# Performance work log

Hardware: AMD Instinct MI355X
Metric: run time of the kernel (lower is better)

The kernel has to match this reference:

```python
import jax, jax.numpy as jnp
import numpy as np

IMPOSSIBLE = -10000.0
TAGSET_SIZE = 64
NUM_TAGS = TAGSET_SIZE + 2  # C = 66
START_IDX = NUM_TAGS - 2
STOP_IDX = NUM_TAGS - 1
B, L, D = 32, 1024, 1024


def setup_inputs() -> dict:
    key = jax.random.key(0)
    k1, k2, k3, k4, k5 = jax.random.split(key, 5)
    features = jax.random.normal(k1, (B, L, D), dtype=jnp.float32)
    ys = jax.random.randint(k2, (B, L), 0, TAGSET_SIZE).astype(jnp.int64)
    masks = jnp.ones((B, L), dtype=jnp.float32)
    fc_w = jax.random.normal(k3, (D, NUM_TAGS), dtype=jnp.float32) / np.sqrt(D)
    fc_b = jax.random.normal(k4, (NUM_TAGS,), dtype=jnp.float32) * 0.01
    transitions = jax.random.normal(k5, (NUM_TAGS, NUM_TAGS), dtype=jnp.float32)
    # transitions TO start and FROM stop are impossible (torch indexing [to, from])
    transitions = transitions.at[START_IDX, :].set(IMPOSSIBLE)
    transitions = transitions.at[:, STOP_IDX].set(IMPOSSIBLE)
    return {"features": features, "ys": ys, "masks": masks,
            "fc_w": fc_w, "fc_b": fc_b, "transitions": transitions}


def _forward_algorithm(feats, masks, transitions):
    """CRF partition function. feats: [B,L,C], masks: [B,L] -> [B]."""
    Bb, Ll, C = feats.shape
    scores0 = jnp.full((Bb, C), IMPOSSIBLE, dtype=feats.dtype).at[:, START_IDX].set(0.0)

    def step(scores, xs):
        emit_t, m_t = xs  # emit_t: [B,C], m_t: [B]
        # score_t[b, j] = logsumexp_i( scores[b,i] + trans[j,i] + emit[b,j] )
        score_t = jax.nn.logsumexp(
            scores[:, None, :] + transitions[None, :, :] + emit_t[:, :, None], axis=-1)
        scores = score_t * m_t[:, None] + scores * (1.0 - m_t[:, None])
        return scores, None

    xs = (jnp.swapaxes(feats, 0, 1), jnp.swapaxes(masks, 0, 1))  # [L,B,C], [L,B]
    scores, _ = jax.lax.scan(step, scores0, xs)
    return jax.nn.logsumexp(scores + transitions[STOP_IDX][None, :], axis=-1)


def _score_sentence(feats, tags, masks, transitions):
    """Score of the gold tag path. feats: [B,L,C], tags: [B,L] -> [B]."""
    Bb, Ll, C = feats.shape
    emit = jnp.take_along_axis(feats, tags[:, :, None], axis=2)[:, :, 0]  # [B,L]
    start = jnp.full((Bb, 1), START_IDX, dtype=tags.dtype)
    tags_ext = jnp.concatenate([start, tags], axis=1)  # [B,L+1]
    trans_sc = transitions[tags_ext[:, 1:], tags_ext[:, :-1]]  # [B,L]
    lengths = masks.sum(1).astype(jnp.int32)  # [B]
    last_tag = tags_ext[jnp.arange(Bb), lengths]  # [B]
    last_score = transitions[STOP_IDX, last_tag]
    return ((trans_sc + emit) * masks).sum(1) + last_score


def reference(features, ys, masks, fc_w, fc_b, transitions):
    feats = jnp.einsum('bld,dc->blc', features, fc_w) + fc_b  # [B,L,C]
    masks_ = masks.astype(feats.dtype)
    forward_score = _forward_algorithm(feats, masks_, transitions)  # [B]
    gold_score = _score_sentence(feats, ys.astype(jnp.int32), masks_, transitions)  # [B]
    return (forward_score, gold_score)
```

## Files before the change

kernel.cpp:

```cpp
#include <hip/hip_runtime.h>
#include <hip/hip_bf16.h>
#include <stdint.h>


#define START_IDX 64
#define STOP_IDX 65
#define LN2F 0.6931471805599453f

typedef __attribute__((ext_vector_type(4))) float f32x4;
typedef __attribute__((ext_vector_type(8))) __bf16 bf16x8;
typedef __attribute__((ext_vector_type(4))) __bf16 bf16x4;

template <int CTRL>
__device__ __forceinline__ float dpp_mov(float v) {
  return __int_as_float(
      __builtin_amdgcn_update_dpp(0, __float_as_int(v), CTRL, 0xF, 0xF, true));
}
__device__ __forceinline__ float wave_max64(float v) {
  v = fmaxf(v, dpp_mov<0xB1>(v));
  v = fmaxf(v, dpp_mov<0x4E>(v));
  v = fmaxf(v, dpp_mov<0x141>(v));
  v = fmaxf(v, dpp_mov<0x140>(v));
  v = fmaxf(v, dpp_mov<0x142>(v));
  v = fmaxf(v, dpp_mov<0x143>(v));
  return v;
}
__device__ __forceinline__ float wave_sum64(float v) {
  v += dpp_mov<0xB1>(v);
  v += dpp_mov<0x4E>(v);
  v += dpp_mov<0x141>(v);
  v += dpp_mov<0x140>(v);
  v += dpp_mov<0x142>(v);
  v += dpp_mov<0x143>(v);
  return v;
}

__global__ void crf_wcvt(const float* __restrict__ W,
                         unsigned short* __restrict__ Wbt) {
  const int idx = blockIdx.x * 256 + threadIdx.x;
  const int n = idx >> 10, k = idx & 1023;
  union { __bf16 h; unsigned short u; } cv;
  cv.h = (__bf16)W[k * 66 + n];
  Wbt[idx] = cv.u;
}

__global__ __launch_bounds__(256) void crf_mm(const float* __restrict__ A,
                                              const unsigned short* __restrict__ Wbt,
                                              const float* __restrict__ bias,
                                              float* __restrict__ out) {
  const int tid = threadIdx.x;
  const int w = tid >> 6, lane = tid & 63, g = lane >> 4, q = lane & 15;
  const int m0 = blockIdx.x * 64 + 16 * w;

  const float* Arow = A + (size_t)(m0 + q) * 1024 + 8 * g;
  const unsigned short* Bp0 = Wbt + (q + 0) * 1024 + 8 * g;
  const unsigned short* Bp1 = Wbt + (q + 16) * 1024 + 8 * g;
  const unsigned short* Bp2 = Wbt + (q + 32) * 1024 + 8 * g;
  const unsigned short* Bp3 = Wbt + (q + 48) * 1024 + 8 * g;

  f32x4 acc0 = {0.f, 0.f, 0.f, 0.f}, acc1 = acc0, acc2 = acc0, acc3 = acc0;

#pragma unroll
  for (int k0 = 0; k0 < 1024; k0 += 32) {
    float4 a0 = *(const float4*)(Arow + k0);
    float4 a1 = *(const float4*)(Arow + k0 + 4);
    bf16x8 af;
    af[0] = (__bf16)a0.x; af[1] = (__bf16)a0.y; af[2] = (__bf16)a0.z; af[3] = (__bf16)a0.w;
    af[4] = (__bf16)a1.x; af[5] = (__bf16)a1.y; af[6] = (__bf16)a1.z; af[7] = (__bf16)a1.w;
    bf16x8 b0 = *(const bf16x8*)(Bp0 + k0);
    bf16x8 b1 = *(const bf16x8*)(Bp1 + k0);
    bf16x8 b2 = *(const bf16x8*)(Bp2 + k0);
    bf16x8 b3 = *(const bf16x8*)(Bp3 + k0);
    acc0 = __builtin_amdgcn_mfma_f32_16x16x32_bf16(af, b0, acc0, 0, 0, 0);
    acc1 = __builtin_amdgcn_mfma_f32_16x16x32_bf16(af, b1, acc1, 0, 0, 0);
    acc2 = __builtin_amdgcn_mfma_f32_16x16x32_bf16(af, b2, acc2, 0, 0, 0);
    acc3 = __builtin_amdgcn_mfma_f32_16x16x32_bf16(af, b3, acc3, 0, 0, 0);
  }

  const float bb0 = bias[q + 0], bb1 = bias[q + 16];
  const float bb2 = bias[q + 32], bb3 = bias[q + 48];
#pragma unroll
  for (int r = 0; r < 4; ++r) {
    float* orow = out + (size_t)(m0 + 4 * g + r) * 64 + q;
    orow[0]  = acc0[r] + bb0;
    orow[16] = acc1[r] + bb1;
    orow[32] = acc2[r] + bb2;
    orow[48] = acc3[r] + bb3;
  }
}

__global__ __launch_bounds__(256) void crf_chunks(const float* __restrict__ feats,
                                                  const float* __restrict__ masks,
                                                  const float* __restrict__ trans,
                                                  float* __restrict__ chunkP,
                                                  int* __restrict__ chunkExp) {
  __shared__ __align__(16) unsigned short T[2][4096];
  __shared__ float wmax[2][4];
  const int tid = threadIdx.x;
  const int w = tid >> 6, lane = tid & 63, g = lane >> 4, q = lane & 15;
  const int c = blockIdx.x, b = blockIdx.y;
  const int t0 = (c == 0) ? 1 : (c << 6);
  const int t1 = (c << 6) + 64;

  bf16x8 Ea0, Ea1;
  {
    const int i = 16 * w + q;
    const float* tp0 = trans + i * 66 + 8 * g;
    const float* tp1 = tp0 + 32;
#pragma unroll
    for (int e = 0; e < 8; ++e) {
      Ea0[e] = (__bf16)__expf(tp0[e]);
      Ea1[e] = (__bf16)__expf(tp1[e]);
    }
  }

  for (int idx = tid; idx < 4096; idx += 256) {
    const int n = idx >> 6, mm = idx & 63;
    const int off = n * 128 + ((2 * mm) ^ ((n & 7) << 4));
    *(unsigned short*)((char*)T[0] + off) =
        (n == mm) ? (unsigned short)0x3F80 : (unsigned short)0;
  }
  if (tid < 4) wmax[0][tid] = 1.0f;

  float pv[4][4];
#pragma unroll
  for (int nt = 0; nt < 4; ++nt)
#pragma unroll
    for (int r = 0; r < 4; ++r)
      pv[nt][r] = ((16 * w + 4 * g + r) == (q + 16 * nt)) ? 1.f : 0.f;

  const float* fb = feats + ((size_t)b << 16);
  const float* mb = masks + (b << 10);
  const int tml = t0 + lane;
  const float mkv = mb[tml > 1023 ? 1023 : tml];

  int e_acc = 0;
  int cur = 0;
  __syncthreads();

  const int ecol = 16 * w + 4 * g;
  float4 fa = *(const float4*)(fb + t0 * 64 + ecol);
  int tpre = t0 + 1; if (tpre > 1023) tpre = 1023;
  float4 fbv = *(const float4*)(fb + tpre * 64 + ecol);

  for (int t = t0; t < t1; ++t) {
    int tn = t + 2; if (tn > 1023) tn = 1023;
    float4 fnext = *(const float4*)(fb + tn * 64 + ecol);
    float4 fcur = fa; fa = fbv; fbv = fnext;
    const float m =
        __int_as_float(__builtin_amdgcn_readlane(__float_as_int(mkv), t - t0));
    if (m != 0.f) {
      const char* Tb = (const char*)T[cur];
      f32x4 acc[4];
#pragma unroll
      for (int nt = 0; nt < 4; ++nt) {
        const int n = q + 16 * nt;
        const int sw = (n & 7) << 4;
        bf16x8 B0 = *(const bf16x8*)(Tb + n * 128 + ((16 * g) ^ sw));
        bf16x8 B1 = *(const bf16x8*)(Tb + n * 128 + ((64 + 16 * g) ^ sw));
        f32x4 z = {0.f, 0.f, 0.f, 0.f};
        z = __builtin_amdgcn_mfma_f32_16x16x32_bf16(Ea0, B0, z, 0, 0, 0);
        acc[nt] = __builtin_amdgcn_mfma_f32_16x16x32_bf16(Ea1, B1, acc[nt] = z, 0, 0, 0);
      }
      const float4 wm = *(const float4*)wmax[cur];
      const float mx = fmaxf(fmaxf(wm.x, wm.y), fmaxf(wm.z, wm.w));
      const int ex = ((__float_as_int(mx) >> 23) & 0xFF) - 127;
      const float sc = __int_as_float((127 - ex) << 23);
      float ce[4];
      ce[0] = __expf(fcur.x) * sc; ce[1] = __expf(fcur.y) * sc;
      ce[2] = __expf(fcur.z) * sc; ce[3] = __expf(fcur.w) * sc;
      float lm = 0.f;
#pragma unroll
      for (int nt = 0; nt < 4; ++nt) {
#pragma unroll
        for (int r = 0; r < 4; ++r) {
          float val = acc[nt][r] * ce[r];
          if (m != 1.f) val = m * val + (1.f - m) * sc * pv[nt][r];
          pv[nt][r] = val;
          lm = fmaxf(lm, val);
        }
      }
      lm = wave_max64(lm);
      const int nxt = cur ^ 1;
      char* Tw = (char*)T[nxt];
#pragma unroll
      for (int nt = 0; nt < 4; ++nt) {
        bf16x4 o;
        o[0] = (__bf16)pv[nt][0]; o[1] = (__bf16)pv[nt][1];
        o[2] = (__bf16)pv[nt][2]; o[3] = (__bf16)pv[nt][3];
        const int n = q + 16 * nt;
        *(bf16x4*)(Tw + n * 128 + ((32 * w + 8 * g) ^ ((n & 7) << 4))) = o;
      }
      if (lane == 63) wmax[nxt][w] = lm;
      e_acc += ex;
      __syncthreads();
      cur = nxt;
    }
  }

#pragma unroll
  for (int nt = 0; nt < 4; ++nt)
#pragma unroll
    for (int r = 0; r < 4; ++r)
      chunkP[(((size_t)(b * 16 + c)) << 12) + (size_t)(16 * w + 4 * g + r) * 64 +
             q + 16 * nt] = pv[nt][r];
  if (tid == 0) chunkExp[b * 16 + c] = e_acc;
}

__global__ void crf_combine(const float* __restrict__ feats,
                            const float* __restrict__ trans,
                            const float* __restrict__ chunkP,
                            const int* __restrict__ chunkExp,
                            float* __restrict__ out) {
  __shared__ __align__(16) float vb[64];
  const int lane = threadIdx.x;
  const int b = blockIdx.x;
  float v = __expf(feats[((size_t)b << 16) + lane]) *
            __expf(trans[lane * 66 + START_IDX]);
  int e_acc = 0;
  for (int c = 0; c < 16; ++c) {
    vb[lane] = v;
    __builtin_amdgcn_wave_barrier();
    const float* Pr = chunkP + (((size_t)(b * 16 + c)) << 12) + (size_t)lane * 64;
    float q0 = 0.f, q1 = 0.f, q2 = 0.f, q3 = 0.f;
#pragma unroll
    for (int j4 = 0; j4 < 16; ++j4) {
      float4 p = *(const float4*)(Pr + 4 * j4);
      float4 x = ((const float4*)vb)[j4];
      q0 = fmaf(p.x, x.x, q0); q1 = fmaf(p.y, x.y, q1);
      q2 = fmaf(p.z, x.z, q2); q3 = fmaf(p.w, x.w, q3);
    }
    const float qq = (q0 + q1) + (q2 + q3);
    float mx = wave_max64(qq);
    mx = __int_as_float(__builtin_amdgcn_readlane(__float_as_int(mx), 63));
    const int ex = ((__float_as_int(mx) >> 23) & 0xFF) - 127;
    v = qq * __int_as_float((127 - ex) << 23);
    e_acc += ex + chunkExp[b * 16 + c];
    __builtin_amdgcn_wave_barrier();
  }
  const float sum = wave_sum64(v * __expf(trans[STOP_IDX * 66 + lane]));
  const float s = __int_as_float(__builtin_amdgcn_readlane(__float_as_int(sum), 63));
  if (lane == 0) out[b] = __logf(s) + (float)e_acc * LN2F;
}

__global__ void crf_gold(const float* __restrict__ fw,
                         const int* __restrict__ ys,
                         const float* __restrict__ masks,
                         const float* __restrict__ trans,
                         float* __restrict__ out) {
  const int lane = threadIdx.x;
  const int b = blockIdx.x;
  const float* fb = fw + (size_t)b * (1024 * 64);
  const float* mb = masks + b * 1024;
  const int* yb = ys + b * 1024;
  float s = 0.f, cnt = 0.f;
#pragma unroll
  for (int c = 0; c < 16; ++c) {
    const int t = c * 64 + lane;
    const float m = mb[t];
    const int y = yb[t];
    const int yp = (t == 0) ? START_IDX : yb[t - 1];
    s += (trans[y * 66 + yp] + fb[t * 64 + y]) * m;
    cnt += m;
  }
  float tot = wave_sum64(s);
  float len = wave_sum64(cnt);
  int totb = __builtin_amdgcn_readlane(__float_as_int(tot), 63);
  int lenb = __builtin_amdgcn_readlane(__float_as_int(len), 63);
  if (lane == 0) {
    const int Lr = (int)__int_as_float(lenb);
    const int last = (Lr == 0) ? START_IDX : yb[Lr - 1];
    out[32 + b] = __int_as_float(totb) + trans[STOP_IDX * 66 + last];
  }
}

extern "C" void kernel_launch(void* const* d_in, const int* in_sizes, int n_in,
                              void* d_out, int out_size, void* d_ws, size_t ws_size,
                              hipStream_t stream) {
  const float* features = (const float*)d_in[0];
  const int* ys         = (const int*)d_in[1];
  const float* masks    = (const float*)d_in[2];
  const float* fc_w     = (const float*)d_in[3];
  const float* fc_b     = (const float*)d_in[4];
  const float* trans    = (const float*)d_in[5];
  float* outp = (float*)d_out;

  char* ws = (char*)d_ws;
  float* feats_ws = (float*)ws;
  unsigned short* Wbt = (unsigned short*)(ws + 8388608);
  float* chunkP = (float*)(ws + 8388608 + 131072);
  int* chunkExp = (int*)(ws + 8388608 + 131072 + 8388608);

  crf_wcvt<<<256, 256, 0, stream>>>(fc_w, Wbt);
  crf_mm<<<512, 256, 0, stream>>>(features, Wbt, fc_b, feats_ws);
  dim3 cg(16, 32);
  crf_chunks<<<cg, 256, 0, stream>>>(feats_ws, masks, trans, chunkP, chunkExp);
  crf_combine<<<32, 64, 0, stream>>>(feats_ws, trans, chunkP, chunkExp, outp);
  crf_gold<<<32, 64, 0, stream>>>(feats_ws, ys, masks, trans, outp);
}
```

Measured before the change: 304.8 us.

## Fuse projection GEMM into chunk kernel and merge combine with gold scoring

Each (chunk, batch) block of the forward kernel now computes its own 64x64 tile of emission logits with MFMA, writes them to the workspace for later use, and caches exp(emissions) in shared memory. The scan loop reads that cache instead of reloading feats from global memory and recomputing exp on every step. The combine and gold-score kernels are merged into a single launch, with even blocks doing the combine and odd blocks doing the gold score. This removes two launches and the global round-trip of emissions into the scan, at the cost of 16 KB of extra LDS per block and only 512 blocks to run the GEMM.

```diff
diff --git a/kernel.cpp b/kernel.cpp
--- a/kernel.cpp
+++ b/kernel.cpp
@@ -44,63 +44,68 @@
   Wbt[idx] = cv.u;
 }
 
-__global__ __launch_bounds__(256) void crf_mm(const float* __restrict__ A,
-                                              const unsigned short* __restrict__ Wbt,
-                                              const float* __restrict__ bias,
-                                              float* __restrict__ out) {
-  const int tid = threadIdx.x;
-  const int w = tid >> 6, lane = tid & 63, g = lane >> 4, q = lane & 15;
-  const int m0 = blockIdx.x * 64 + 16 * w;
-
-  const float* Arow = A + (size_t)(m0 + q) * 1024 + 8 * g;
-  const unsigned short* Bp0 = Wbt + (q + 0) * 1024 + 8 * g;
-  const unsigned short* Bp1 = Wbt + (q + 16) * 1024 + 8 * g;
-  const unsigned short* Bp2 = Wbt + (q + 32) * 1024 + 8 * g;
-  const unsigned short* Bp3 = Wbt + (q + 48) * 1024 + 8 * g;
-
-  f32x4 acc0 = {0.f, 0.f, 0.f, 0.f}, acc1 = acc0, acc2 = acc0, acc3 = acc0;
-
-#pragma unroll
-  for (int k0 = 0; k0 < 1024; k0 += 32) {
-    float4 a0 = *(const float4*)(Arow + k0);
-    float4 a1 = *(const float4*)(Arow + k0 + 4);
-    bf16x8 af;
-    af[0] = (__bf16)a0.x; af[1] = (__bf16)a0.y; af[2] = (__bf16)a0.z; af[3] = (__bf16)a0.w;
-    af[4] = (__bf16)a1.x; af[5] = (__bf16)a1.y; af[6] = (__bf16)a1.z; af[7] = (__bf16)a1.w;
-    bf16x8 b0 = *(const bf16x8*)(Bp0 + k0);
-    bf16x8 b1 = *(const bf16x8*)(Bp1 + k0);
-    bf16x8 b2 = *(const bf16x8*)(Bp2 + k0);
-    bf16x8 b3 = *(const bf16x8*)(Bp3 + k0);
-    acc0 = __builtin_amdgcn_mfma_f32_16x16x32_bf16(af, b0, acc0, 0, 0, 0);
-    acc1 = __builtin_amdgcn_mfma_f32_16x16x32_bf16(af, b1, acc1, 0, 0, 0);
-    acc2 = __builtin_amdgcn_mfma_f32_16x16x32_bf16(af, b2, acc2, 0, 0, 0);
-    acc3 = __builtin_amdgcn_mfma_f32_16x16x32_bf16(af, b3, acc3, 0, 0, 0);
-  }
-
-  const float bb0 = bias[q + 0], bb1 = bias[q + 16];
-  const float bb2 = bias[q + 32], bb3 = bias[q + 48];
-#pragma unroll
-  for (int r = 0; r < 4; ++r) {
-    float* orow = out + (size_t)(m0 + 4 * g + r) * 64 + q;
-    orow[0]  = acc0[r] + bb0;
-    orow[16] = acc1[r] + bb1;
-    orow[32] = acc2[r] + bb2;
-    orow[48] = acc3[r] + bb3;
-  }
-}
-
-__global__ __launch_bounds__(256) void crf_chunks(const float* __restrict__ feats,
-                                                  const float* __restrict__ masks,
-                                                  const float* __restrict__ trans,
-                                                  float* __restrict__ chunkP,
-                                                  int* __restrict__ chunkExp) {
+__global__ __launch_bounds__(256) void crf_fwd(const float* __restrict__ features,
+                                               const unsigned short* __restrict__ Wbt,
+                                               const float* __restrict__ bias,
+                                               const float* __restrict__ masks,
+                                               const float* __restrict__ trans,
+                                               float* __restrict__ featsOut,
+                                               float* __restrict__ chunkP,
+                                               int* __restrict__ chunkExp) {
+  __shared__ __align__(16) float expE[64][64];
   __shared__ __align__(16) unsigned short T[2][4096];
   __shared__ float wmax[2][4];
   const int tid = threadIdx.x;
   const int w = tid >> 6, lane = tid & 63, g = lane >> 4, q = lane & 15;
   const int c = blockIdx.x, b = blockIdx.y;
-  const int t0 = (c == 0) ? 1 : (c << 6);
-  const int t1 = (c << 6) + 64;
+
+  for (int idx = tid; idx < 4096; idx += 256) {
+    const int n = idx >> 6, mm = idx & 63;
+    const int off = n * 128 + ((2 * mm) ^ ((n & 7) << 4));
+    *(unsigned short*)((char*)T[0] + off) =
+        (n == mm) ? (unsigned short)0x3F80 : (unsigned short)0;
+  }
+  if (tid < 4) wmax[0][tid] = 1.0f;
+
+  {
+    const int trow = (c << 6) + 16 * w + q;
+    const float* Arow = features + ((size_t)b << 20) + (size_t)trow * 1024 + 8 * g;
+    const unsigned short* Bp0 = Wbt + (q + 0) * 1024 + 8 * g;
+    const unsigned short* Bp1 = Wbt + (q + 16) * 1024 + 8 * g;
+    const unsigned short* Bp2 = Wbt + (q + 32) * 1024 + 8 * g;
+    const unsigned short* Bp3 = Wbt + (q + 48) * 1024 + 8 * g;
+    f32x4 acc0 = {0.f, 0.f, 0.f, 0.f}, acc1 = acc0, acc2 = acc0, acc3 = acc0;
+#pragma unroll
+    for (int k0 = 0; k0 < 1024; k0 += 32) {
+      float4 a0 = *(const float4*)(Arow + k0);
+      float4 a1 = *(const float4*)(Arow + k0 + 4);
+      bf16x8 af;
+      af[0] = (__bf16)a0.x; af[1] = (__bf16)a0.y; af[2] = (__bf16)a0.z; af[3] = (__bf16)a0.w;
+      af[4] = (__bf16)a1.x; af[5] = (__bf16)a1.y; af[6] = (__bf16)a1.z; af[7] = (__bf16)a1.w;
+      bf16x8 b0 = *(const bf16x8*)(Bp0 + k0);
+      bf16x8 b1 = *(const bf16x8*)(Bp1 + k0);
+      bf16x8 b2 = *(const bf16x8*)(Bp2 + k0);
+      bf16x8 b3 = *(const bf16x8*)(Bp3 + k0);
+      acc0 = __builtin_amdgcn_mfma_f32_16x16x32_bf16(af, b0, acc0, 0, 0, 0);
+      acc1 = __builtin_amdgcn_mfma_f32_16x16x32_bf16(af, b1, acc1, 0, 0, 0);
+      acc2 = __builtin_amdgcn_mfma_f32_16x16x32_bf16(af, b2, acc2, 0, 0, 0);
+      acc3 = __builtin_amdgcn_mfma_f32_16x16x32_bf16(af, b3, acc3, 0, 0, 0);
+    }
+    const float bb0 = bias[q + 0], bb1 = bias[q + 16];
+    const float bb2 = bias[q + 32], bb3 = bias[q + 48];
+#pragma unroll
+    for (int r = 0; r < 4; ++r) {
+      const int tl = 16 * w + 4 * g + r;
+      float* orow = featsOut + (((size_t)(b << 10) + (c << 6) + tl) << 6) + q;
+      const float v0 = acc0[r] + bb0, v1 = acc1[r] + bb1;
+      const float v2 = acc2[r] + bb2, v3 = acc3[r] + bb3;
+      orow[0] = v0; orow[16] = v1; orow[32] = v2; orow[48] = v3;
+      expE[tl][q + 0]  = __expf(v0);
+      expE[tl][q + 16] = __expf(v1);
+      expE[tl][q + 32] = __expf(v2);
+      expE[tl][q + 48] = __expf(v3);
+    }
+  }
 
   bf16x8 Ea0, Ea1;
   {
@@ -114,14 +119,6 @@
     }
   }
 
-  for (int idx = tid; idx < 4096; idx += 256) {
-    const int n = idx >> 6, mm = idx & 63;
-    const int off = n * 128 + ((2 * mm) ^ ((n & 7) << 4));
-    *(unsigned short*)((char*)T[0] + off) =
-        (n == mm) ? (unsigned short)0x3F80 : (unsigned short)0;
-  }
-  if (tid < 4) wmax[0][tid] = 1.0f;
-
   float pv[4][4];
 #pragma unroll
   for (int nt = 0; nt < 4; ++nt)
@@ -129,7 +126,8 @@
     for (int r = 0; r < 4; ++r)
       pv[nt][r] = ((16 * w + 4 * g + r) == (q + 16 * nt)) ? 1.f : 0.f;
 
-  const float* fb = feats + ((size_t)b << 16);
+  const int t0 = (c == 0) ? 1 : (c << 6);
+  const int t1 = (c << 6) + 64;
   const float* mb = masks + (b << 10);
   const int tml = t0 + lane;
   const float mkv = mb[tml > 1023 ? 1023 : tml];
@@ -138,15 +136,9 @@
   int cur = 0;
   __syncthreads();
 
-  const int ecol = 16 * w + 4 * g;
-  float4 fa = *(const float4*)(fb + t0 * 64 + ecol);
-  int tpre = t0 + 1; if (tpre > 1023) tpre = 1023;
-  float4 fbv = *(const float4*)(fb + tpre * 64 + ecol);
-
   for (int t = t0; t < t1; ++t) {
-    int tn = t + 2; if (tn > 1023) tn = 1023;
-    float4 fnext = *(const float4*)(fb + tn * 64 + ecol);
-    float4 fcur = fa; fa = fbv; fbv = fnext;
+    const int tl = t - (c << 6);
+    const float4 ee = *(const float4*)&expE[tl][16 * w + 4 * g];
     const float m =
         __int_as_float(__builtin_amdgcn_readlane(__float_as_int(mkv), t - t0));
     if (m != 0.f) {
@@ -160,15 +152,14 @@
         bf16x8 B1 = *(const bf16x8*)(Tb + n * 128 + ((64 + 16 * g) ^ sw));
         f32x4 z = {0.f, 0.f, 0.f, 0.f};
         z = __builtin_amdgcn_mfma_f32_16x16x32_bf16(Ea0, B0, z, 0, 0, 0);
-        acc[nt] = __builtin_amdgcn_mfma_f32_16x16x32_bf16(Ea1, B1, acc[nt] = z, 0, 0, 0);
+        acc[nt] = __builtin_amdgcn_mfma_f32_16x16x32_bf16(Ea1, B1, z, 0, 0, 0);
       }
       const float4 wm = *(const float4*)wmax[cur];
       const float mx = fmaxf(fmaxf(wm.x, wm.y), fmaxf(wm.z, wm.w));
       const int ex = ((__float_as_int(mx) >> 23) & 0xFF) - 127;
       const float sc = __int_as_float((127 - ex) << 23);
       float ce[4];
-      ce[0] = __expf(fcur.x) * sc; ce[1] = __expf(fcur.y) * sc;
-      ce[2] = __expf(fcur.z) * sc; ce[3] = __expf(fcur.w) * sc;
+      ce[0] = ee.x * sc; ce[1] = ee.y * sc; ce[2] = ee.z * sc; ce[3] = ee.w * sc;
       float lm = 0.f;
 #pragma unroll
       for (int nt = 0; nt < 4; ++nt) {
@@ -207,70 +198,67 @@
   if (tid == 0) chunkExp[b * 16 + c] = e_acc;
 }
 
-__global__ void crf_combine(const float* __restrict__ feats,
-                            const float* __restrict__ trans,
-                            const float* __restrict__ chunkP,
-                            const int* __restrict__ chunkExp,
-                            float* __restrict__ out) {
+__global__ void crf_fin(const float* __restrict__ feats,
+                        const int* __restrict__ ys,
+                        const float* __restrict__ masks,
+                        const float* __restrict__ trans,
+                        const float* __restrict__ chunkP,
+                        const int* __restrict__ chunkExp,
+                        float* __restrict__ out) {
   __shared__ __align__(16) float vb[64];
   const int lane = threadIdx.x;
-  const int b = blockIdx.x;
-  float v = __expf(feats[((size_t)b << 16) + lane]) *
-            __expf(trans[lane * 66 + START_IDX]);
-  int e_acc = 0;
-  for (int c = 0; c < 16; ++c) {
-    vb[lane] = v;
-    __builtin_amdgcn_wave_barrier();
-    const float* Pr = chunkP + (((size_t)(b * 16 + c)) << 12) + (size_t)lane * 64;
-    float q0 = 0.f, q1 = 0.f, q2 = 0.f, q3 = 0.f;
-#pragma unroll
-    for (int j4 = 0; j4 < 16; ++j4) {
-      float4 p = *(const float4*)(Pr + 4 * j4);
-      float4 x = ((const float4*)vb)[j4];
-      q0 = fmaf(p.x, x.x, q0); q1 = fmaf(p.y, x.y, q1);
-      q2 = fmaf(p.z, x.z, q2); q3 = fmaf(p.w, x.w, q3);
-    }
-    const float qq = (q0 + q1) + (q2 + q3);
-    float mx = wave_max64(qq);
-    mx = __int_as_float(__builtin_amdgcn_readlane(__float_as_int(mx), 63));
-    const int ex = ((__float_as_int(mx) >> 23) & 0xFF) - 127;
-    v = qq * __int_as_float((127 - ex) << 23);
-    e_acc += ex + chunkExp[b * 16 + c];
-    __builtin_amdgcn_wave_barrier();
-  }
-  const float sum = wave_sum64(v * __expf(trans[STOP_IDX * 66 + lane]));
-  const float s = __int_as_float(__builtin_amdgcn_readlane(__float_as_int(sum), 63));
-  if (lane == 0) out[b] = __logf(s) + (float)e_acc * LN2F;
-}
-
-__global__ void crf_gold(const float* __restrict__ fw,
-                         const int* __restrict__ ys,
-                         const float* __restrict__ masks,
-                         const float* __restrict__ trans,
-                         float* __restrict__ out) {
-  const int lane = threadIdx.x;
-  const int b = blockIdx.x;
-  const float* fb = fw + (size_t)b * (1024 * 64);
-  const float* mb = masks + b * 1024;
-  const int* yb = ys + b * 1024;
-  float s = 0.f, cnt = 0.f;
-#pragma unroll
-  for (int c = 0; c < 16; ++c) {
-    const int t = c * 64 + lane;
-    const float m = mb[t];
-    const int y = yb[t];
-    const int yp = (t == 0) ? START_IDX : yb[t - 1];
-    s += (trans[y * 66 + yp] + fb[t * 64 + y]) * m;
-    cnt += m;
-  }
-  float tot = wave_sum64(s);
-  float len = wave_sum64(cnt);
-  int totb = __builtin_amdgcn_readlane(__float_as_int(tot), 63);
-  int lenb = __builtin_amdgcn_readlane(__float_as_int(len), 63);
-  if (lane == 0) {
-    const int Lr = (int)__int_as_float(lenb);
-    const int last = (Lr == 0) ? START_IDX : yb[Lr - 1];
-    out[32 + b] = __int_as_float(totb) + trans[STOP_IDX * 66 + last];
+  const int b = blockIdx.x >> 1;
+  if ((blockIdx.x & 1) == 0) {
+    float v = __expf(feats[((size_t)b << 16) + lane]) *
+              __expf(trans[lane * 66 + START_IDX]);
+    int e_acc = 0;
+    for (int cc = 0; cc < 16; ++cc) {
+      vb[lane] = v;
+      __builtin_amdgcn_wave_barrier();
+      const float* Pr = chunkP + (((size_t)(b * 16 + cc)) << 12) + (size_t)lane * 64;
+      float q0 = 0.f, q1 = 0.f, q2 = 0.f, q3 = 0.f;
+#pragma unroll
+      for (int j4 = 0; j4 < 16; ++j4) {
+        float4 p = *(const float4*)(Pr + 4 * j4);
+        float4 x = ((const float4*)vb)[j4];
+        q0 = fmaf(p.x, x.x, q0); q1 = fmaf(p.y, x.y, q1);
+        q2 = fmaf(p.z, x.z, q2); q3 = fmaf(p.w, x.w, q3);
+      }
+      const float qq = (q0 + q1) + (q2 + q3);
+      float mx = wave_max64(qq);
+      mx = __int_as_float(__builtin_amdgcn_readlane(__float_as_int(mx), 63));
+      const int ex = ((__float_as_int(mx) >> 23) & 0xFF) - 127;
+      v = qq * __int_as_float((127 - ex) << 23);
+      e_acc += ex + chunkExp[b * 16 + cc];
+      __builtin_amdgcn_wave_barrier();
+    }
+    const float sum = wave_sum64(v * __expf(trans[STOP_IDX * 66 + lane]));
+    const float s =
+        __int_as_float(__builtin_amdgcn_readlane(__float_as_int(sum), 63));
+    if (lane == 0) out[b] = __logf(s) + (float)e_acc * LN2F;
+  } else {
+    const float* fb = feats + ((size_t)b << 16);
+    const float* mb = masks + (b << 10);
+    const int* yb = ys + (b << 10);
+    float s = 0.f, cnt = 0.f;
+#pragma unroll
+    for (int cc = 0; cc < 16; ++cc) {
+      const int t = cc * 64 + lane;
+      const float m = mb[t];
+      const int y = yb[t];
+      const int yp = (t == 0) ? START_IDX : yb[t - 1];
+      s += (trans[y * 66 + yp] + fb[t * 64 + y]) * m;
+      cnt += m;
+    }
+    float tot = wave_sum64(s);
+    float len = wave_sum64(cnt);
+    int totb = __builtin_amdgcn_readlane(__float_as_int(tot), 63);
+    int lenb = __builtin_amdgcn_readlane(__float_as_int(len), 63);
+    if (lane == 0) {
+      const int Lr = (int)__int_as_float(lenb);
+      const int last = (Lr == 0) ? START_IDX : yb[Lr - 1];
+      out[32 + b] = __int_as_float(totb) + trans[STOP_IDX * 66 + last];
+    }
   }
 }
 
@@ -292,9 +280,8 @@
   int* chunkExp = (int*)(ws + 8388608 + 131072 + 8388608);
 
   crf_wcvt<<<256, 256, 0, stream>>>(fc_w, Wbt);
-  crf_mm<<<512, 256, 0, stream>>>(features, Wbt, fc_b, feats_ws);
   dim3 cg(16, 32);
-  crf_chunks<<<cg, 256, 0, stream>>>(feats_ws, masks, trans, chunkP, chunkExp);
-  crf_combine<<<32, 64, 0, stream>>>(feats_ws, trans, chunkP, chunkExp, outp);
-  crf_gold<<<32, 64, 0, stream>>>(feats_ws, ys, masks, trans, outp);
-}
+  crf_fwd<<<cg, 256, 0, stream>>>(features, Wbt, fc_b, masks, trans,
+                                  feats_ws, chunkP, chunkExp);
+  crf_fin<<<64, 64, 0, stream>>>(feats_ws, ys, masks, trans, chunkP, chunkExp, outp);
+}
```

Measured after the change: 285.9 us. 1.07x faster.
